# Performance work log

Hardware: AMD Instinct MI355X
Metric: run time of the kernel (lower is better)

The kernel has to match this reference:

```python
import jax, jax.numpy as jnp
import numpy as np

N_NODES = 50000
N_EDGES = 800000
IN_DIM = 2
EDGE_DIM = 2
HIDDEN = 64
N_LAYERS = 3
MAX_LEAKS = 3


def setup_inputs() -> dict:
    key = jax.random.key(0)
    ks = iter(jax.random.split(key, 32))
    s = 0.05
    inp = {
        "x": jax.random.normal(next(ks), (N_NODES, IN_DIM), dtype=jnp.float32),
        "edge_index": jax.random.randint(next(ks), (2, N_EDGES), 0, N_NODES, dtype=jnp.int32),
        "edge_attr": jax.random.normal(next(ks), (N_EDGES, EDGE_DIM), dtype=jnp.float32),
        # input projection
        "W_in": jax.random.normal(next(ks), (IN_DIM, HIDDEN), dtype=jnp.float32) * s,
        "b_in": jnp.zeros((HIDDEN,), jnp.float32),
        # message-passing layers (stacked over L)
        "W_msg": jax.random.normal(next(ks), (N_LAYERS, HIDDEN + EDGE_DIM, HIDDEN), dtype=jnp.float32) * s,
        "b_msg": jnp.zeros((N_LAYERS, HIDDEN), jnp.float32),
        "W_upd": jax.random.normal(next(ks), (N_LAYERS, 2 * HIDDEN, HIDDEN), dtype=jnp.float32) * s,
        "b_upd": jnp.zeros((N_LAYERS, HIDDEN), jnp.float32),
        # per-node leak-logit head
        "W_node": jax.random.normal(next(ks), (HIDDEN, 1), dtype=jnp.float32) * s,
        "b_node": jnp.zeros((1,), jnp.float32),
        # global no-leak head
        "W_pool": jax.random.normal(next(ks), (HIDDEN, 1), dtype=jnp.float32) * s,
        "b_pool": jnp.zeros((1,), jnp.float32),
        # num_leaks head: Linear(H, H//2) -> ReLU -> Linear(H//2, max_leaks+1)
        "W_h1": jax.random.normal(next(ks), (HIDDEN, HIDDEN // 2), dtype=jnp.float32) * s,
        "b_h1": jnp.zeros((HIDDEN // 2,), jnp.float32),
        "W_h2": jax.random.normal(next(ks), (HIDDEN // 2, MAX_LEAKS + 1), dtype=jnp.float32) * s,
        "b_h2": jnp.zeros((MAX_LEAKS + 1,), jnp.float32),
    }
    return inp


def _run_gnn(x, src, dst, edge_attr, W_in, b_in, W_msg, b_msg, W_upd, b_upd):
    """input_proj + num_layers of message passing; returns node embeddings h [N, H]."""
    n_nodes = x.shape[0]
    h = x @ W_in + b_in  # [N, H]
    # in-degree for mean aggregation (clamped to avoid div-by-zero)
    deg = jax.ops.segment_sum(jnp.ones((src.shape[0],), h.dtype), dst, num_segments=n_nodes)
    deg = jnp.maximum(deg, 1.0)[:, None]  # [N, 1]
    for l in range(N_LAYERS):
        # message: MLP over [h_src || edge_attr], gathered along edges
        m = jax.nn.relu(jnp.concatenate([h[src], edge_attr], axis=-1) @ W_msg[l] + b_msg[l])  # [E, H]
        agg = jax.ops.segment_sum(m, dst, num_segments=n_nodes) / deg  # [N, H]
        # update: MLP over [h || agg]
        h = jax.nn.relu(jnp.concatenate([h, agg], axis=-1) @ W_upd[l] + b_upd[l])  # [N, H]
    return h


def reference(x, edge_index, edge_attr, W_in, b_in, W_msg, b_msg, W_upd, b_upd,
              W_node, b_node, W_pool, b_pool, W_h1, b_h1, W_h2, b_h2):
    src, dst = edge_index[0], edge_index[1]
    # base GNN forward (dropout is identity at inference)
    h = _run_gnn(x, src, dst, edge_attr, W_in, b_in, W_msg, b_msg, W_upd, b_upd)  # [N, H]
    node_logits = (h @ W_node + b_node)[:, 0]          # [N]
    node_probs = jax.nn.sigmoid(node_logits)           # [N]
    # the multi-leak forward re-runs input_proj + mp_layers; identical math -> reuse h
    h_global = jnp.mean(h, axis=0, keepdims=True)      # [1, H]
    num_leaks_logits = jax.nn.relu(h_global @ W_h1 + b_h1) @ W_h2 + b_h2  # [1, max_leaks+1]
    return node_probs, num_leaks_logits, h
```

## Files before the change

kernel.cpp:

```cpp
#include <hip/hip_runtime.h>
#include <math.h>

constexpr int H = 64;

typedef __attribute__((ext_vector_type(8))) short bf16x8;
typedef __attribute__((ext_vector_type(4))) float f32x4;
typedef unsigned long long u64;

__device__ inline unsigned short f2bf(float f) {
  union { float f; unsigned int u; } c; c.f = f;
  unsigned int u = c.u;
  return (unsigned short)((u + 0x7FFF + ((u >> 16) & 1)) >> 16);
}
__device__ inline float bf2f(unsigned int s) {
  union { unsigned int u; float f; } c; c.u = s << 16;
  return c.f;
}
__device__ inline unsigned char f2fp8(float f) {
  return (unsigned char)(__builtin_amdgcn_cvt_pk_fp8_f32(f, f, 0, false) & 0xFF);
}

__global__ void k_prep(int* __restrict__ hist, float* __restrict__ hsumP,
                       const float* __restrict__ Wmsg, const float* __restrict__ Wupd,
                       unsigned short* __restrict__ WmT, unsigned short* __restrict__ WuT,
                       int n) {
  int t = blockIdx.x * blockDim.x + threadIdx.x;
  if (t < n) hist[t] = 0;
  if (t < 512) hsumP[t] = 0.f;
  int u = t - n;
  if (u >= 0 && u < 3 * 12288) {
    int l = u / 12288, rem = u % 12288;
    if (rem < 4096) {
      int j = rem >> 6, k = rem & 63;
      WmT[l * 4096 + rem] = f2bf(Wmsg[(size_t)l * 66 * 64 + k * 64 + j]);
    } else {
      int r2 = rem - 4096;
      int j = r2 >> 7, k = r2 & 127;
      WuT[l * 8192 + r2] = f2bf(Wupd[(size_t)l * 128 * 64 + k * 64 + j]);
    }
  }
}

__global__ void k_hist(const int* __restrict__ dst, int* __restrict__ hist, int E) {
  int e = blockIdx.x * blockDim.x + threadIdx.x;
  if (e < E) atomicAdd(&hist[dst[e]], 1);
}

__global__ void k_scan1(const int* __restrict__ hist, int* __restrict__ bsum, int n) {
  __shared__ int sred[256];
  int tid = threadIdx.x;
  int base = blockIdx.x * 1024 + tid * 4;
  int s = 0;
#pragma unroll
  for (int k = 0; k < 4; ++k) { int i = base + k; if (i < n) s += hist[i]; }
  sred[tid] = s;
  __syncthreads();
  for (int d = 128; d > 0; d >>= 1) {
    if (tid < d) sred[tid] += sred[tid + d];
    __syncthreads();
  }
  if (tid == 0) bsum[blockIdx.x] = sred[0];
}

__global__ void k_scan2(int* __restrict__ bsum, int* __restrict__ bcur, int nb) {
  __shared__ int sd[1024];
  int tid = threadIdx.x;
  int v = (tid < nb) ? bsum[tid] : 0;
  sd[tid] = v;
  __syncthreads();
  for (int d = 1; d < 1024; d <<= 1) {
    int t = (tid >= d) ? sd[tid - d] : 0;
    __syncthreads();
    sd[tid] += t;
    __syncthreads();
  }
  if (tid < nb) {
    int ex = sd[tid] - v;
    bsum[tid] = ex;
    bcur[tid] = ex;
  }
}

__global__ void k_scan3(const int* __restrict__ hist, const int* __restrict__ bsum,
                        int* __restrict__ row_ptr, int* __restrict__ pos, int n) {
  __shared__ int sth[256];
  int tid = threadIdx.x;
  int base = blockIdx.x * 1024 + tid * 4;
  int v[4]; int s = 0;
#pragma unroll
  for (int k = 0; k < 4; ++k) { int i = base + k; v[k] = (i < n) ? hist[i] : 0; s += v[k]; }
  sth[tid] = s;
  __syncthreads();
  for (int d = 1; d < 256; d <<= 1) {
    int t = (tid >= d) ? sth[tid - d] : 0;
    __syncthreads();
    sth[tid] += t;
    __syncthreads();
  }
  int run = bsum[blockIdx.x] + sth[tid] - s;
  if (blockIdx.x == 0 && tid == 0) row_ptr[0] = 0;
#pragma unroll
  for (int k = 0; k < 4; ++k) {
    int i = base + k;
    if (i < n) {
      pos[i] = run;
      run += v[k];
      row_ptr[i + 1] = run;
    }
  }
}

__global__ void k_part(const int* __restrict__ src, const int* __restrict__ dst,
                       const float2* __restrict__ ea2, int* __restrict__ bcur,
                       u64* __restrict__ staged, int E, int B) {
  __shared__ u64 srt[2048];
  __shared__ int cnt[64], offs[64], gbase[64];
  int tid = threadIdx.x;
  int base = blockIdx.x * 2048;
  if (tid < 64) cnt[tid] = 0;
  __syncthreads();
  u64 rec_[8]; int bk_[8], rk_[8];
#pragma unroll
  for (int k = 0; k < 8; ++k) {
    int e = base + k * 256 + tid;
    if (e < E) {
      int d = dst[e];
      int bk = d >> 10;
      float2 eav = ea2[e];
      unsigned int eap = (unsigned int)f2bf(eav.x) | ((unsigned int)f2bf(eav.y) << 16);
      rec_[k] = (u64)(unsigned int)(src[e] & 0xFFFF)
              | ((u64)(unsigned int)(d & 1023) << 16)
              | ((u64)(unsigned int)bk << 26)
              | ((u64)eap << 32);
      bk_[k] = bk;
      rk_[k] = atomicAdd(&cnt[bk], 1);
    } else bk_[k] = -1;
  }
  __syncthreads();
  if (tid == 0) {
    int run = 0;
    for (int b = 0; b < B; ++b) { offs[b] = run; run += cnt[b]; }
  }
  __syncthreads();
#pragma unroll
  for (int k = 0; k < 8; ++k)
    if (bk_[k] >= 0) srt[offs[bk_[k]] + rk_[k]] = rec_[k];
  __syncthreads();
  if (tid < B && cnt[tid] > 0) gbase[tid] = atomicAdd(&bcur[tid], cnt[tid]);
  __syncthreads();
  int total = (base + 2048 <= E) ? 2048 : (E > base ? E - base : 0);
  for (int i = tid; i < total; i += 256) {
    u64 r = srt[i];
    int bk = (int)((r >> 26) & 63u);
    staged[gbase[bk] + (i - offs[bk])] = r;
  }
}

__global__ void k_place(const u64* __restrict__ staged, const int* __restrict__ rptr,
                        u64* __restrict__ erec, int N_) {
  __shared__ int cnt2[1024];
  __shared__ int rptrL[1025];
  int b = blockIdx.x;
  int nd0 = b << 10;
  int nn = min(nd0 + 1024, N_) - nd0;
  int tid = threadIdx.x;
  if (tid < nn) { cnt2[tid] = 0; rptrL[tid] = rptr[nd0 + tid]; }
  if (tid == 0) rptrL[nn] = rptr[nd0 + nn];
  __syncthreads();
  int beg = rptrL[0], end = rptrL[nn];
  for (int i = beg + tid; i < end; i += 1024) {
    u64 r = staged[i];
    int dl = (int)((r >> 16) & 1023u);
    int p = rptrL[dl] + atomicAdd(&cnt2[dl], 1);
    erec[p] = (r & 0xFFFFull) | ((r >> 32) << 32);
  }
}

__global__ void k_scatter(const int* __restrict__ src, const int* __restrict__ dst,
                          const float* __restrict__ ea, int* __restrict__ pos,
                          u64* __restrict__ erec, int E) {
  int e = blockIdx.x * blockDim.x + threadIdx.x;
  if (e < E) {
    int d = dst[e];
    int p = atomicAdd(&pos[d], 1);
    u64 lo = f2bf(ea[2 * e]);
    u64 hi = f2bf(ea[2 * e + 1]);
    erec[p] = (u64)(unsigned int)src[e] | ((lo | (hi << 16)) << 32);
  }
}

__global__ void k_inproj_gemm(const float* __restrict__ x, const float* __restrict__ Win,
                              const float* __restrict__ bin,
                              const unsigned short* __restrict__ wmt,
                              unsigned short* __restrict__ hb,
                              unsigned char* __restrict__ g, int n) {
  int lane = threadIdx.x & 63;
  int wv = blockIdx.x * (blockDim.x >> 6) + (threadIdx.x >> 6);
  int v0 = wv * 16;
  if (v0 >= n) return;
  int r16 = lane & 15, hi = lane >> 4;
  int row = v0 + r16;
  float x0 = 0.f, x1 = 0.f;
  if (row < n) { x0 = x[2 * row]; x1 = x[2 * row + 1]; }
  union { bf16x8 v; unsigned short u[8]; } af[2];
#pragma unroll
  for (int s = 0; s < 2; ++s)
#pragma unroll
    for (int t = 0; t < 8; ++t) {
      int j = s * 32 + hi * 8 + t;
      af[s].u[t] = f2bf(fmaf(x0, Win[j], fmaf(x1, Win[64 + j], bin[j])));
    }
  if (row < n) {
    *(bf16x8*)(hb + (size_t)row * H + hi * 8)      = af[0].v;
    *(bf16x8*)(hb + (size_t)row * H + 32 + hi * 8) = af[1].v;
  }
  bf16x8 bfr[2][4];
#pragma unroll
  for (int ks = 0; ks < 2; ++ks)
#pragma unroll
    for (int jt = 0; jt < 4; ++jt)
      bfr[ks][jt] = *(const bf16x8*)(wmt + (jt * 16 + r16) * 64 + ks * 32 + hi * 8);
  f32x4 acc[4] = {};
#pragma unroll
  for (int ks = 0; ks < 2; ++ks)
#pragma unroll
    for (int jt = 0; jt < 4; ++jt)
      acc[jt] = __builtin_amdgcn_mfma_f32_16x16x32_bf16(af[ks].v, bfr[ks][jt], acc[jt], 0, 0, 0);
#pragma unroll
  for (int jt = 0; jt < 4; ++jt) {
    int col = jt * 16 + r16;
#pragma unroll
    for (int r = 0; r < 4; ++r) {
      int orow = v0 + hi * 4 + r;
      if (orow < n) g[(size_t)orow * H + col] = f2fp8(acc[jt][r]);
    }
  }
}

__device__ inline void acc8(float* a, uint2 gw, float e0, float e1,
                            const float4 waL, const float4 waH,
                            const float4 wbL, const float4 wbH,
                            const float4 bL, const float4 bH) {
  a[0] += fmaxf(fmaf(e0, waL.x, fmaf(e1, wbL.x, __builtin_amdgcn_cvt_f32_fp8(gw.x, 0) + bL.x)), 0.f);
  a[1] += fmaxf(fmaf(e0, waL.y, fmaf(e1, wbL.y, __builtin_amdgcn_cvt_f32_fp8(gw.x, 1) + bL.y)), 0.f);
  a[2] += fmaxf(fmaf(e0, waL.z, fmaf(e1, wbL.z, __builtin_amdgcn_cvt_f32_fp8(gw.x, 2) + bL.z)), 0.f);
  a[3] += fmaxf(fmaf(e0, waL.w, fmaf(e1, wbL.w, __builtin_amdgcn_cvt_f32_fp8(gw.x, 3) + bL.w)), 0.f);
  a[4] += fmaxf(fmaf(e0, waH.x, fmaf(e1, wbH.x, __builtin_amdgcn_cvt_f32_fp8(gw.y, 0) + bH.x)), 0.f);
  a[5] += fmaxf(fmaf(e0, waH.y, fmaf(e1, wbH.y, __builtin_amdgcn_cvt_f32_fp8(gw.y, 1) + bH.y)), 0.f);
  a[6] += fmaxf(fmaf(e0, waH.z, fmaf(e1, wbH.z, __builtin_amdgcn_cvt_f32_fp8(gw.y, 2) + bH.z)), 0.f);
  a[7] += fmaxf(fmaf(e0, waH.w, fmaf(e1, wbH.w, __builtin_amdgcn_cvt_f32_fp8(gw.y, 3) + bH.w)), 0.f);
}

__global__ void k_agg(const unsigned char* __restrict__ g, const int* __restrict__ row_ptr,
                      const u64* __restrict__ erec,
                      const float* __restrict__ Wm2, const float* __restrict__ bm,
                      unsigned short* __restrict__ aggb, int n) {
  int r = threadIdx.x & 7;
  int j0 = r * 8;
  float4 waL = *(const float4*)(Wm2 + j0);
  float4 waH = *(const float4*)(Wm2 + j0 + 4);
  float4 wbL = *(const float4*)(Wm2 + 64 + j0);
  float4 wbH = *(const float4*)(Wm2 + 64 + j0 + 4);
  float4 bL  = *(const float4*)(bm + j0);
  float4 bH  = *(const float4*)(bm + j0 + 4);
  int v = blockIdx.x * (blockDim.x >> 3) + (threadIdx.x >> 3);
  if (v >= n) return;
  int beg = row_ptr[v], end = row_ptr[v + 1];
  float a[8] = {0.f, 0.f, 0.f, 0.f, 0.f, 0.f, 0.f, 0.f};
  int i = beg;
  for (; i + 3 < end; i += 4) {
    u64 rA = erec[i], rB = erec[i + 1], rC = erec[i + 2], rD = erec[i + 3];
    uint2 gwA = *(const uint2*)(g + (size_t)(unsigned int)rA * H + j0);
    uint2 gwB = *(const uint2*)(g + (size_t)(unsigned int)rB * H + j0);
    uint2 gwC = *(const uint2*)(g + (size_t)(unsigned int)rC * H + j0);
    uint2 gwD = *(const uint2*)(g + (size_t)(unsigned int)rD * H + j0);
    unsigned int eA = (unsigned int)(rA >> 32), eB = (unsigned int)(rB >> 32);
    unsigned int eC = (unsigned int)(rC >> 32), eD = (unsigned int)(rD >> 32);
    acc8(a, gwA, bf2f(eA & 0xffffu), bf2f(eA >> 16), waL, waH, wbL, wbH, bL, bH);
    acc8(a, gwB, bf2f(eB & 0xffffu), bf2f(eB >> 16), waL, waH, wbL, wbH, bL, bH);
    acc8(a, gwC, bf2f(eC & 0xffffu), bf2f(eC >> 16), waL, waH, wbL, wbH, bL, bH);
    acc8(a, gwD, bf2f(eD & 0xffffu), bf2f(eD >> 16), waL, waH, wbL, wbH, bL, bH);
  }
  for (; i < end; ++i) {
    u64 rA = erec[i];
    uint2 gwA = *(const uint2*)(g + (size_t)(unsigned int)rA * H + j0);
    unsigned int eA = (unsigned int)(rA >> 32);
    acc8(a, gwA, bf2f(eA & 0xffffu), bf2f(eA >> 16), waL, waH, wbL, wbH, bL, bH);
  }
  float inv = 1.f / fmaxf((float)(end - beg), 1.f);
  uint4 o;
  o.x = (unsigned int)f2bf(a[0] * inv) | ((unsigned int)f2bf(a[1] * inv) << 16);
  o.y = (unsigned int)f2bf(a[2] * inv) | ((unsigned int)f2bf(a[3] * inv) << 16);
  o.z = (unsigned int)f2bf(a[4] * inv) | ((unsigned int)f2bf(a[5] * inv) << 16);
  o.w = (unsigned int)f2bf(a[6] * inv) | ((unsigned int)f2bf(a[7] * inv) << 16);
  *(uint4*)(aggb + (size_t)v * H + j0) = o;
}

__global__ void k_updgemm(const unsigned short* __restrict__ hb,
                          const unsigned short* __restrict__ aggb,
                          const unsigned short* __restrict__ wut,
                          const float* __restrict__ bu,
                          const unsigned short* __restrict__ wmt_next,
                          unsigned short* __restrict__ hb_out,
                          unsigned char* __restrict__ g_out,
                          float* __restrict__ hout,
                          const float* __restrict__ Wn, const float* __restrict__ bn,
                          float* __restrict__ probs, float* __restrict__ hsumP,
                          int n) {
  __shared__ __align__(16) unsigned short hstage[4][16][72];
  __shared__ float shsum[64];
  int lane = threadIdx.x & 63;
  int w = threadIdx.x >> 6;
  int wv = blockIdx.x * (blockDim.x >> 6) + w;
  int v0 = wv * 16;
  bool act = v0 < n;
  int r16 = lane & 15, hi = lane >> 4;
  if (hout && threadIdx.x < 64) shsum[threadIdx.x] = 0.f;
  bf16x8 bfr[4][4];
#pragma unroll
  for (int ks = 0; ks < 4; ++ks)
#pragma unroll
    for (int jt = 0; jt < 4; ++jt)
      bfr[ks][jt] = *(const bf16x8*)(wut + (jt * 16 + r16) * 128 + ks * 32 + hi * 8);
  f32x4 acc[4];
#pragma unroll
  for (int jt = 0; jt < 4; ++jt) {
    float b = bu[jt * 16 + r16];
    acc[jt] = (f32x4){b, b, b, b};
  }
  bf16x8 afr[4];
  int row = v0 + r16;
  if (act && row < n) {
    const unsigned short* hrow = hb   + (size_t)row * H + hi * 8;
    const unsigned short* arow = aggb + (size_t)row * H + hi * 8;
    afr[0] = *(const bf16x8*)(hrow);
    afr[1] = *(const bf16x8*)(hrow + 32);
    afr[2] = *(const bf16x8*)(arow);
    afr[3] = *(const bf16x8*)(arow + 32);
  } else {
    afr[0] = afr[1] = afr[2] = afr[3] = (bf16x8){0,0,0,0,0,0,0,0};
  }
#pragma unroll
  for (int ks = 0; ks < 4; ++ks)
#pragma unroll
    for (int jt = 0; jt < 4; ++jt)
      acc[jt] = __builtin_amdgcn_mfma_f32_16x16x32_bf16(afr[ks], bfr[ks][jt], acc[jt], 0, 0, 0);
  float ov[4][4];
  unsigned short ob[4][4];
#pragma unroll
  for (int jt = 0; jt < 4; ++jt) {
    int col = jt * 16 + r16;
#pragma unroll
    for (int r = 0; r < 4; ++r) {
      int orow = v0 + hi * 4 + r;
      bool ok = act && orow < n;
      float o = fmaxf(acc[jt][r], 0.f);
      ov[jt][r] = ok ? o : 0.f;
      ob[jt][r] = f2bf(ov[jt][r]);
      if (ok) {
        hb_out[(size_t)orow * H + col] = ob[jt][r];
        if (hout) hout[(size_t)orow * H + col] = o;
      }
    }
  }
  if (wmt_next) {
#pragma unroll
    for (int jt = 0; jt < 4; ++jt)
#pragma unroll
      for (int r = 0; r < 4; ++r)
        hstage[w][hi * 4 + r][jt * 16 + r16] = ob[jt][r];
    __syncthreads();
    bf16x8 af2[2];
    af2[0] = *(const bf16x8*)(&hstage[w][r16][hi * 8]);
    af2[1] = *(const bf16x8*)(&hstage[w][r16][32 + hi * 8]);
    bf16x8 bf2r[2][4];
#pragma unroll
    for (int ks = 0; ks < 2; ++ks)
#pragma unroll
      for (int jt = 0; jt < 4; ++jt)
        bf2r[ks][jt] = *(const bf16x8*)(wmt_next + (jt * 16 + r16) * 64 + ks * 32 + hi * 8);
    f32x4 acc2[4] = {};
#pragma unroll
    for (int ks = 0; ks < 2; ++ks)
#pragma unroll
      for (int jt = 0; jt < 4; ++jt)
        acc2[jt] = __builtin_amdgcn_mfma_f32_16x16x32_bf16(af2[ks], bf2r[ks][jt], acc2[jt], 0, 0, 0);
#pragma unroll
    for (int jt = 0; jt < 4; ++jt) {
      int col = jt * 16 + r16;
#pragma unroll
      for (int r = 0; r < 4; ++r) {
        int orow = v0 + hi * 4 + r;
        if (act && orow < n) g_out[(size_t)orow * H + col] = f2fp8(acc2[jt][r]);
      }
    }
  } else {
    float bn0 = bn[0];
    float lg[4] = {0.f, 0.f, 0.f, 0.f};
#pragma unroll
    for (int jt = 0; jt < 4; ++jt) {
      float wn = Wn[jt * 16 + r16];
#pragma unroll
      for (int r = 0; r < 4; ++r) lg[r] = fmaf(ov[jt][r], wn, lg[r]);
    }
#pragma unroll
    for (int d = 1; d < 16; d <<= 1) {
#pragma unroll
      for (int r = 0; r < 4; ++r) lg[r] += __shfl_xor(lg[r], d);
    }
    if (r16 == 0) {
#pragma unroll
      for (int r = 0; r < 4; ++r) {
        int orow = v0 + hi * 4 + r;
        if (act && orow < n) probs[orow] = 1.f / (1.f + expf(-(lg[r] + bn0)));
      }
    }
    __syncthreads();
#pragma unroll
    for (int jt = 0; jt < 4; ++jt) {
      float s = ov[jt][0] + ov[jt][1] + ov[jt][2] + ov[jt][3];
      s += __shfl_xor(s, 16); s += __shfl_xor(s, 32);
      if (hi == 0) atomicAdd(&shsum[jt * 16 + r16], s);
    }
    __syncthreads();
    if (threadIdx.x < 64)
      atomicAdd(&hsumP[((blockIdx.x & 7) << 6) + threadIdx.x], shsum[threadIdx.x]);
  }
}

__global__ void k_final(const float* __restrict__ hsumP,
                        const float* __restrict__ W1, const float* __restrict__ b1,
                        const float* __restrict__ W2, const float* __restrict__ b2,
                        float* __restrict__ out4, float n_nodes) {
  __shared__ float hmean[64];
  __shared__ float z1[32];
  int tid = threadIdx.x;
  if (tid < 64) {
    float s = 0.f;
#pragma unroll
    for (int b = 0; b < 8; ++b) s += hsumP[b * 64 + tid];
    hmean[tid] = s / n_nodes;
  }
  __syncthreads();
  if (tid < 32) {
    float a = b1[tid];
    for (int k = 0; k < 64; ++k) a = fmaf(hmean[k], W1[k * 32 + tid], a);
    z1[tid] = fmaxf(a, 0.f);
  }
  __syncthreads();
  if (tid < 4) {
    float a = b2[tid];
    for (int k = 0; k < 32; ++k) a = fmaf(z1[k], W2[k * 4 + tid], a);
    out4[tid] = a;
  }
}

extern "C" void kernel_launch(void* const* d_in, const int* in_sizes, int n_in,
                              void* d_out, int out_size, void* d_ws, size_t ws_size,
                              hipStream_t stream) {
  const float* x    = (const float*)d_in[0];
  const int*   ei   = (const int*)d_in[1];
  const float* ea   = (const float*)d_in[2];
  const float* Win  = (const float*)d_in[3];
  const float* bin  = (const float*)d_in[4];
  const float* Wmsg = (const float*)d_in[5];
  const float* bmsg = (const float*)d_in[6];
  const float* Wupd = (const float*)d_in[7];
  const float* bupd = (const float*)d_in[8];
  const float* Wn   = (const float*)d_in[9];
  const float* bn   = (const float*)d_in[10];
  const float* W1   = (const float*)d_in[13];
  const float* b1   = (const float*)d_in[14];
  const float* W2   = (const float*)d_in[15];
  const float* b2   = (const float*)d_in[16];

  const int N = in_sizes[0] / 2;
  const int E = in_sizes[1] / 2;
  const int* src = ei;
  const int* dst = ei + E;

  char* ws = (char*)d_ws;
  size_t off = 0;
  auto alloc = [&](size_t bytes) {
    void* p = ws + off;
    off = (off + bytes + 255) & ~(size_t)255;
    return p;
  };
  int*   hist = (int*)  alloc((size_t)N * 4);
  int*   rptr = (int*)  alloc((size_t)(N + 1) * 4);
  int*   pos  = (int*)  alloc((size_t)N * 4);
  int*   bsum = (int*)  alloc((size_t)1024 * 4);
  int*   bcur = (int*)  alloc((size_t)1024 * 4);
  u64*   staged = (u64*)alloc((size_t)E * 8);
  u64*   erec = (u64*)  alloc((size_t)E * 8);
  unsigned short* hb   = (unsigned short*)alloc((size_t)N * H * 2);
  unsigned char*  g    = (unsigned char*) alloc((size_t)N * H);
  unsigned short* aggb = (unsigned short*)alloc((size_t)N * H * 2);
  unsigned short* WmT  = (unsigned short*)alloc((size_t)3 * 64 * 64 * 2);
  unsigned short* WuT  = (unsigned short*)alloc((size_t)3 * 64 * 128 * 2);
  float* hsumP = (float*)alloc(8 * 64 * 4);
  (void)ws_size;

  float* probs = (float*)d_out;
  float* out4  = probs + N;
  float* h     = out4 + 4;

  int eb = (E + 255) / 256;
  int sb = (N + 1023) / 1024;
  k_prep<<<(N + 3 * 12288 + 255) / 256, 256, 0, stream>>>(hist, hsumP, Wmsg, Wupd, WmT, WuT, N);
  k_hist<<<eb, 256, 0, stream>>>(dst, hist, E);
  k_scan1<<<sb, 256, 0, stream>>>(hist, bsum, N);
  k_scan2<<<1, 1024, 0, stream>>>(bsum, bcur, sb);
  k_scan3<<<sb, 256, 0, stream>>>(hist, bsum, rptr, pos, N);

  int B = (N + 1023) >> 10;
  if (B <= 64) {
    k_part<<<(E + 2047) / 2048, 256, 0, stream>>>(src, dst, (const float2*)ea,
                                                  bcur, staged, E, B);
    k_place<<<B, 1024, 0, stream>>>(staged, rptr, erec, N);
  } else {
    k_scatter<<<eb, 256, 0, stream>>>(src, dst, ea, pos, erec, E);
  }

  int tiles = (N + 15) / 16;
  int mb = (tiles + 3) / 4;
  k_inproj_gemm<<<mb, 256, 0, stream>>>(x, Win, bin, WmT, hb, g, N);

  int ab = (N + 31) / 32;
  for (int l = 0; l < 3; ++l) {
    k_agg<<<ab, 256, 0, stream>>>(g, rptr, erec,
                                  Wmsg + (size_t)l * 66 * 64 + 64 * 64,
                                  bmsg + (size_t)l * 64, aggb, N);
    k_updgemm<<<mb, 256, 0, stream>>>(hb, aggb, WuT + (size_t)l * 64 * 128,
                                      bupd + (size_t)l * 64,
                                      (l < 2) ? (WmT + (size_t)(l + 1) * 64 * 64) : nullptr,
                                      hb, g,
                                      (l == 2) ? h : nullptr,
                                      Wn, bn, probs, hsumP, N);
  }

  k_final<<<1, 64, 0, stream>>>(hsumP, W1, b1, W2, b2, out4, (float)N);
}
```

Baseline: 219.0 us.

## Fuse edge aggregation and update GEMM into one per-layer kernel

The separate aggregation and update-GEMM kernels are merged into one k_layer kernel. Each 256-thread block aggregates messages for 64 nodes into shared memory and then runs the MFMA update on those rows. This removes the global bf16 agg buffer round trip and one launch per layer. To avoid a read/write race on the fp8 message-projection buffer between blocks, it is now double-buffered (gA/gB). The fused kernel carries more shared memory and registers, and GEMM warps wait at a barrier on the slowest aggregation group, which may reduce occupancy.

```diff
diff --git a/kernel.cpp b/kernel.cpp
--- a/kernel.cpp
+++ b/kernel.cpp
@@ -251,70 +251,77 @@
   a[7] += fmaxf(fmaf(e0, waH.w, fmaf(e1, wbH.w, __builtin_amdgcn_cvt_f32_fp8(gw.y, 3) + bH.w)), 0.f);
 }
 
-__global__ void k_agg(const unsigned char* __restrict__ g, const int* __restrict__ row_ptr,
-                      const u64* __restrict__ erec,
-                      const float* __restrict__ Wm2, const float* __restrict__ bm,
-                      unsigned short* __restrict__ aggb, int n) {
-  int r = threadIdx.x & 7;
-  int j0 = r * 8;
-  float4 waL = *(const float4*)(Wm2 + j0);
-  float4 waH = *(const float4*)(Wm2 + j0 + 4);
-  float4 wbL = *(const float4*)(Wm2 + 64 + j0);
-  float4 wbH = *(const float4*)(Wm2 + 64 + j0 + 4);
-  float4 bL  = *(const float4*)(bm + j0);
-  float4 bH  = *(const float4*)(bm + j0 + 4);
-  int v = blockIdx.x * (blockDim.x >> 3) + (threadIdx.x >> 3);
-  if (v >= n) return;
-  int beg = row_ptr[v], end = row_ptr[v + 1];
-  float a[8] = {0.f, 0.f, 0.f, 0.f, 0.f, 0.f, 0.f, 0.f};
-  int i = beg;
-  for (; i + 3 < end; i += 4) {
-    u64 rA = erec[i], rB = erec[i + 1], rC = erec[i + 2], rD = erec[i + 3];
-    uint2 gwA = *(const uint2*)(g + (size_t)(unsigned int)rA * H + j0);
-    uint2 gwB = *(const uint2*)(g + (size_t)(unsigned int)rB * H + j0);
-    uint2 gwC = *(const uint2*)(g + (size_t)(unsigned int)rC * H + j0);
-    uint2 gwD = *(const uint2*)(g + (size_t)(unsigned int)rD * H + j0);
-    unsigned int eA = (unsigned int)(rA >> 32), eB = (unsigned int)(rB >> 32);
-    unsigned int eC = (unsigned int)(rC >> 32), eD = (unsigned int)(rD >> 32);
-    acc8(a, gwA, bf2f(eA & 0xffffu), bf2f(eA >> 16), waL, waH, wbL, wbH, bL, bH);
-    acc8(a, gwB, bf2f(eB & 0xffffu), bf2f(eB >> 16), waL, waH, wbL, wbH, bL, bH);
-    acc8(a, gwC, bf2f(eC & 0xffffu), bf2f(eC >> 16), waL, waH, wbL, wbH, bL, bH);
-    acc8(a, gwD, bf2f(eD & 0xffffu), bf2f(eD >> 16), waL, waH, wbL, wbH, bL, bH);
-  }
-  for (; i < end; ++i) {
-    u64 rA = erec[i];
-    uint2 gwA = *(const uint2*)(g + (size_t)(unsigned int)rA * H + j0);
-    unsigned int eA = (unsigned int)(rA >> 32);
-    acc8(a, gwA, bf2f(eA & 0xffffu), bf2f(eA >> 16), waL, waH, wbL, wbH, bL, bH);
-  }
-  float inv = 1.f / fmaxf((float)(end - beg), 1.f);
-  uint4 o;
-  o.x = (unsigned int)f2bf(a[0] * inv) | ((unsigned int)f2bf(a[1] * inv) << 16);
-  o.y = (unsigned int)f2bf(a[2] * inv) | ((unsigned int)f2bf(a[3] * inv) << 16);
-  o.z = (unsigned int)f2bf(a[4] * inv) | ((unsigned int)f2bf(a[5] * inv) << 16);
-  o.w = (unsigned int)f2bf(a[6] * inv) | ((unsigned int)f2bf(a[7] * inv) << 16);
-  *(uint4*)(aggb + (size_t)v * H + j0) = o;
-}
-
-__global__ void k_updgemm(const unsigned short* __restrict__ hb,
-                          const unsigned short* __restrict__ aggb,
-                          const unsigned short* __restrict__ wut,
-                          const float* __restrict__ bu,
-                          const unsigned short* __restrict__ wmt_next,
-                          unsigned short* __restrict__ hb_out,
-                          unsigned char* __restrict__ g_out,
-                          float* __restrict__ hout,
-                          const float* __restrict__ Wn, const float* __restrict__ bn,
-                          float* __restrict__ probs, float* __restrict__ hsumP,
-                          int n) {
+__global__ void k_layer(const unsigned char* __restrict__ g_in,
+                        const int* __restrict__ row_ptr, const u64* __restrict__ erec,
+                        const float* __restrict__ Wm2, const float* __restrict__ bm,
+                        unsigned short* __restrict__ hb,
+                        const unsigned short* __restrict__ wut,
+                        const float* __restrict__ bu,
+                        const unsigned short* __restrict__ wmt_next,
+                        unsigned char* __restrict__ g_out,
+                        float* __restrict__ hout,
+                        const float* __restrict__ Wn, const float* __restrict__ bn,
+                        float* __restrict__ probs, float* __restrict__ hsumP,
+                        int n) {
+  __shared__ __align__(16) unsigned short aggL[64][72];
   __shared__ __align__(16) unsigned short hstage[4][16][72];
   __shared__ float shsum[64];
+  int v0 = blockIdx.x * 64;
+
+  {
+    int gid = threadIdx.x >> 3, r = threadIdx.x & 7;
+    int j0 = r * 8;
+    float4 waL = *(const float4*)(Wm2 + j0);
+    float4 waH = *(const float4*)(Wm2 + j0 + 4);
+    float4 wbL = *(const float4*)(Wm2 + 64 + j0);
+    float4 wbH = *(const float4*)(Wm2 + 64 + j0 + 4);
+    float4 bL  = *(const float4*)(bm + j0);
+    float4 bH  = *(const float4*)(bm + j0 + 4);
+#pragma unroll
+    for (int it = 0; it < 2; ++it) {
+      int lv = it * 32 + gid;
+      int v = v0 + lv;
+      uint4 o = make_uint4(0, 0, 0, 0);
+      if (v < n) {
+        int beg = row_ptr[v], end = row_ptr[v + 1];
+        float a[8] = {0.f, 0.f, 0.f, 0.f, 0.f, 0.f, 0.f, 0.f};
+        int i = beg;
+        for (; i + 3 < end; i += 4) {
+          u64 rA = erec[i], rB = erec[i + 1], rC = erec[i + 2], rD = erec[i + 3];
+          uint2 gwA = *(const uint2*)(g_in + (size_t)(unsigned int)rA * H + j0);
+          uint2 gwB = *(const uint2*)(g_in + (size_t)(unsigned int)rB * H + j0);
+          uint2 gwC = *(const uint2*)(g_in + (size_t)(unsigned int)rC * H + j0);
+          uint2 gwD = *(const uint2*)(g_in + (size_t)(unsigned int)rD * H + j0);
+          unsigned int eA = (unsigned int)(rA >> 32), eB = (unsigned int)(rB >> 32);
+          unsigned int eC = (unsigned int)(rC >> 32), eD = (unsigned int)(rD >> 32);
+          acc8(a, gwA, bf2f(eA & 0xffffu), bf2f(eA >> 16), waL, waH, wbL, wbH, bL, bH);
+          acc8(a, gwB, bf2f(eB & 0xffffu), bf2f(eB >> 16), waL, waH, wbL, wbH, bL, bH);
+          acc8(a, gwC, bf2f(eC & 0xffffu), bf2f(eC >> 16), waL, waH, wbL, wbH, bL, bH);
+          acc8(a, gwD, bf2f(eD & 0xffffu), bf2f(eD >> 16), waL, waH, wbL, wbH, bL, bH);
+        }
+        for (; i < end; ++i) {
+          u64 rA = erec[i];
+          uint2 gwA = *(const uint2*)(g_in + (size_t)(unsigned int)rA * H + j0);
+          unsigned int eA = (unsigned int)(rA >> 32);
+          acc8(a, gwA, bf2f(eA & 0xffffu), bf2f(eA >> 16), waL, waH, wbL, wbH, bL, bH);
+        }
+        float inv = 1.f / fmaxf((float)(end - beg), 1.f);
+        o.x = (unsigned int)f2bf(a[0] * inv) | ((unsigned int)f2bf(a[1] * inv) << 16);
+        o.y = (unsigned int)f2bf(a[2] * inv) | ((unsigned int)f2bf(a[3] * inv) << 16);
+        o.z = (unsigned int)f2bf(a[4] * inv) | ((unsigned int)f2bf(a[5] * inv) << 16);
+        o.w = (unsigned int)f2bf(a[6] * inv) | ((unsigned int)f2bf(a[7] * inv) << 16);
+      }
+      *(uint4*)(&aggL[lv][j0]) = o;
+    }
+  }
+  __syncthreads();
+
   int lane = threadIdx.x & 63;
   int w = threadIdx.x >> 6;
-  int wv = blockIdx.x * (blockDim.x >> 6) + w;
-  int v0 = wv * 16;
-  bool act = v0 < n;
+  int wv0 = v0 + w * 16;
+  bool act = wv0 < n;
   int r16 = lane & 15, hi = lane >> 4;
+  int lw = w * 16 + r16;
   if (hout && threadIdx.x < 64) shsum[threadIdx.x] = 0.f;
   bf16x8 bfr[4][4];
 #pragma unroll
@@ -329,17 +336,16 @@
     acc[jt] = (f32x4){b, b, b, b};
   }
   bf16x8 afr[4];
-  int row = v0 + r16;
+  int row = wv0 + r16;
   if (act && row < n) {
-    const unsigned short* hrow = hb   + (size_t)row * H + hi * 8;
-    const unsigned short* arow = aggb + (size_t)row * H + hi * 8;
+    const unsigned short* hrow = hb + (size_t)row * H + hi * 8;
     afr[0] = *(const bf16x8*)(hrow);
     afr[1] = *(const bf16x8*)(hrow + 32);
-    afr[2] = *(const bf16x8*)(arow);
-    afr[3] = *(const bf16x8*)(arow + 32);
   } else {
-    afr[0] = afr[1] = afr[2] = afr[3] = (bf16x8){0,0,0,0,0,0,0,0};
-  }
+    afr[0] = afr[1] = (bf16x8){0,0,0,0,0,0,0,0};
+  }
+  afr[2] = *(const bf16x8*)(&aggL[lw][hi * 8]);
+  afr[3] = *(const bf16x8*)(&aggL[lw][32 + hi * 8]);
 #pragma unroll
   for (int ks = 0; ks < 4; ++ks)
 #pragma unroll
@@ -352,13 +358,13 @@
     int col = jt * 16 + r16;
 #pragma unroll
     for (int r = 0; r < 4; ++r) {
-      int orow = v0 + hi * 4 + r;
+      int orow = wv0 + hi * 4 + r;
       bool ok = act && orow < n;
       float o = fmaxf(acc[jt][r], 0.f);
       ov[jt][r] = ok ? o : 0.f;
       ob[jt][r] = f2bf(ov[jt][r]);
       if (ok) {
-        hb_out[(size_t)orow * H + col] = ob[jt][r];
+        hb[(size_t)orow * H + col] = ob[jt][r];
         if (hout) hout[(size_t)orow * H + col] = o;
       }
     }
@@ -390,7 +396,7 @@
       int col = jt * 16 + r16;
 #pragma unroll
       for (int r = 0; r < 4; ++r) {
-        int orow = v0 + hi * 4 + r;
+        int orow = wv0 + hi * 4 + r;
         if (act && orow < n) g_out[(size_t)orow * H + col] = f2fp8(acc2[jt][r]);
       }
     }
@@ -411,7 +417,7 @@
     if (r16 == 0) {
 #pragma unroll
       for (int r = 0; r < 4; ++r) {
-        int orow = v0 + hi * 4 + r;
+        int orow = wv0 + hi * 4 + r;
         if (act && orow < n) probs[orow] = 1.f / (1.f + expf(-(lg[r] + bn0)));
       }
     }
@@ -494,8 +500,8 @@
   u64*   staged = (u64*)alloc((size_t)E * 8);
   u64*   erec = (u64*)  alloc((size_t)E * 8);
   unsigned short* hb   = (unsigned short*)alloc((size_t)N * H * 2);
-  unsigned char*  g    = (unsigned char*) alloc((size_t)N * H);
-  unsigned short* aggb = (unsigned short*)alloc((size_t)N * H * 2);
+  unsigned char*  gA   = (unsigned char*) alloc((size_t)N * H);
+  unsigned char*  gB   = (unsigned char*) alloc((size_t)N * H);
   unsigned short* WmT  = (unsigned short*)alloc((size_t)3 * 64 * 64 * 2);
   unsigned short* WuT  = (unsigned short*)alloc((size_t)3 * 64 * 128 * 2);
   float* hsumP = (float*)alloc(8 * 64 * 4);
@@ -524,19 +530,21 @@
 
   int tiles = (N + 15) / 16;
   int mb = (tiles + 3) / 4;
-  k_inproj_gemm<<<mb, 256, 0, stream>>>(x, Win, bin, WmT, hb, g, N);
-
-  int ab = (N + 31) / 32;
+  k_inproj_gemm<<<mb, 256, 0, stream>>>(x, Win, bin, WmT, hb, gA, N);
+
+  int lb = (N + 63) / 64;
   for (int l = 0; l < 3; ++l) {
-    k_agg<<<ab, 256, 0, stream>>>(g, rptr, erec,
-                                  Wmsg + (size_t)l * 66 * 64 + 64 * 64,
-                                  bmsg + (size_t)l * 64, aggb, N);
-    k_updgemm<<<mb, 256, 0, stream>>>(hb, aggb, WuT + (size_t)l * 64 * 128,
-                                      bupd + (size_t)l * 64,
-                                      (l < 2) ? (WmT + (size_t)(l + 1) * 64 * 64) : nullptr,
-                                      hb, g,
-                                      (l == 2) ? h : nullptr,
-                                      Wn, bn, probs, hsumP, N);
+    const unsigned char* gin = (l & 1) ? gB : gA;
+    unsigned char* gout      = (l & 1) ? gA : gB;
+    k_layer<<<lb, 256, 0, stream>>>(gin, rptr, erec,
+                                    Wmsg + (size_t)l * 66 * 64 + 64 * 64,
+                                    bmsg + (size_t)l * 64,
+                                    hb, WuT + (size_t)l * 64 * 128,
+                                    bupd + (size_t)l * 64,
+                                    (l < 2) ? (WmT + (size_t)(l + 1) * 64 * 64) : nullptr,
+                                    gout,
+                                    (l == 2) ? h : nullptr,
+                                    Wn, bn, probs, hsumP, N);
   }
 
   k_final<<<1, 64, 0, stream>>>(hsumP, W1, b1, W2, b2, out4, (float)N);
```

Measured after the change: 215.9 us. No clear change (-1.4%).
